# Kernel optimization log

Measured on AMD Instinct MI355X. Metric: run time of the kernel, lower is better.

Reference implementation:

```python
import jax, jax.numpy as jnp
import numpy as np

N_UNITS = 100000
N_EDGES = 1600000
NODE_DIM = 64
N_REL_TYPES = 8
LEAKY_SLOPE = 0.2


def setup_inputs() -> dict:
    key = jax.random.key(0)
    k1, k2, k3, k4, k5 = jax.random.split(key, 5)
    x_unit_base = jax.random.normal(k1, (N_UNITS, NODE_DIM), dtype=jnp.float32)
    hat_t = jax.random.normal(k2, (N_UNITS,), dtype=jnp.float32)
    a_r_params = jax.random.normal(k3, (N_REL_TYPES, 2 * NODE_DIM), dtype=jnp.float32)
    rel_edge_index = jax.random.randint(k4, (2, N_EDGES), 0, N_UNITS, dtype=jnp.int64)
    rel_edge_type = jax.random.randint(k5, (N_EDGES,), 0, N_REL_TYPES, dtype=jnp.int64)
    return {
        "x_unit_base": x_unit_base,
        "hat_t": hat_t,
        "a_r_params": a_r_params,
        "rel_edge_index": rel_edge_index,
        "rel_edge_type": rel_edge_type,
    }


def reference(x_unit_base, hat_t, a_r_params, rel_edge_index, rel_edge_type):
    n_units = x_unit_base.shape[0]
    src = rel_edge_index[0]  # [E]
    dst = rel_edge_index[1]  # [E]

    # Per-edge attention params, split into source/dest halves to avoid
    # materializing the [E, 2d] concat explicitly as a separate buffer.
    a_r = a_r_params[rel_edge_type]          # [E, 2d]
    d = x_unit_base.shape[1]
    a_u, a_v = a_r[:, :d], a_r[:, d:]
    # e = sum(a_r * cat(x_u, x_v)) = <a_u, x_u> + <a_v, x_v>
    e = jnp.sum(a_u * x_unit_base[src], axis=-1) + jnp.sum(a_v * x_unit_base[dst], axis=-1)
    e = jax.nn.leaky_relu(e, negative_slope=LEAKY_SLOPE)  # [E]

    # scatter_softmax over edges grouped by src
    seg_max = jax.ops.segment_max(e, src, num_segments=n_units)  # [N]
    ex = jnp.exp(e - seg_max[src])
    denom = jax.ops.segment_sum(ex, src, num_segments=n_units)   # [N]
    alpha = ex / denom[src]                                       # [E]

    # weighted scatter-sum of imputed treatments
    weighted_t = alpha * hat_t[dst]
    g_u = jax.ops.segment_sum(weighted_t, src, num_segments=n_units)  # [N]
    return g_u[:, None]
```

## Files before the change

### kernel.cpp

```cpp
#include <hip/hip_runtime.h>

#define LEAKY_SLOPE 0.2f
#define SHIFT 20.0f
#define CHUNK 2048
#define LG_CHUNK 11
#define NCH_MAX 64
#define EPB 4096
#define CAP_MIN 34816


__device__ __forceinline__ float lrelu_exp(float a, float b) {
    float e = a + b;
    e = (e > 0.f) ? e : LEAKY_SLOPE * e;
    return __expf(e - SHIFT);
}

template <int NC, bool FUSED>
__global__ __launch_bounds__(256) void node_table_kernel(const float* __restrict__ x,
                                                         const float* __restrict__ a,
                                                         const float* __restrict__ hat_t,
                                                         float* __restrict__ su,
                                                         float* __restrict__ svx,
                                                         float2* __restrict__ nd,
                                                         unsigned* __restrict__ gcur,
                                                         int n_units) {
    int u = blockIdx.x * blockDim.x + threadIdx.x;
    if (blockIdx.x == 0 && threadIdx.x < NCH_MAX && gcur) gcur[threadIdx.x] = 0u;
    if (u >= n_units) return;
#pragma unroll
    for (int k = 0; k < NC; ++k) nd[(size_t)k * n_units + u] = make_float2(0.f, 0.f);

    float4 xr[16];
    const float4* xp = reinterpret_cast<const float4*>(x + (size_t)u * 64);
#pragma unroll
    for (int k = 0; k < 16; ++k) xr[k] = xp[k];

    float out_u[8], out_v[8];
#pragma unroll
    for (int r = 0; r < 8; ++r) {
        const float* ar = a + r * 128;
        float au = 0.f, av = 0.f;
#pragma unroll
        for (int k = 0; k < 16; ++k) {
            float4 xk = xr[k];
            au = fmaf(ar[4 * k + 0], xk.x, au);
            au = fmaf(ar[4 * k + 1], xk.y, au);
            au = fmaf(ar[4 * k + 2], xk.z, au);
            au = fmaf(ar[4 * k + 3], xk.w, au);
            av = fmaf(ar[64 + 4 * k + 0], xk.x, av);
            av = fmaf(ar[64 + 4 * k + 1], xk.y, av);
            av = fmaf(ar[64 + 4 * k + 2], xk.z, av);
            av = fmaf(ar[64 + 4 * k + 3], xk.w, av);
        }
        out_u[r] = au;
        out_v[r] = av;
    }
    float4* sup = reinterpret_cast<float4*>(su + (size_t)u * 8);
    sup[0] = make_float4(out_u[0], out_u[1], out_u[2], out_u[3]);
    sup[1] = make_float4(out_u[4], out_u[5], out_u[6], out_u[7]);
    if (FUSED) {
        float ht = hat_t[u];
        float4* svp = reinterpret_cast<float4*>(svx + (size_t)u * 16);
        svp[0] = make_float4(out_v[0], ht, out_v[1], ht);
        svp[1] = make_float4(out_v[2], ht, out_v[3], ht);
        svp[2] = make_float4(out_v[4], ht, out_v[5], ht);
        svp[3] = make_float4(out_v[6], ht, out_v[7], ht);
    } else {
        float4* svp = reinterpret_cast<float4*>(svx + (size_t)u * 8);
        svp[0] = make_float4(out_v[0], out_v[1], out_v[2], out_v[3]);
        svp[1] = make_float4(out_v[4], out_v[5], out_v[6], out_v[7]);
    }
}

__global__ __launch_bounds__(256) void scatter_kernel(const int* __restrict__ src,
                                                      const int* __restrict__ dst,
                                                      const int* __restrict__ typ,
                                                      unsigned* __restrict__ gcur,
                                                      uint2* __restrict__ buckets,
                                                      int cap, int nch, int n_edges) {
    __shared__ unsigned lcnt[NCH_MAX];
    __shared__ unsigned lbase[NCH_MAX];
    const int tid = threadIdx.x;
    if (tid < NCH_MAX) lcnt[tid] = 0u;
    __syncthreads();

    const int base = blockIdx.x * EPB;
    unsigned pk[16], qk[16], rk[16];
#pragma unroll
    for (int r = 0; r < 4; ++r) {
        int e = base + tid * 4 + r * 1024;
        if (e + 4 <= n_edges) {
            int4 s4 = *reinterpret_cast<const int4*>(src + e);
            int4 d4 = *reinterpret_cast<const int4*>(dst + e);
            int4 t4 = *reinterpret_cast<const int4*>(typ + e);
            int ss[4] = {s4.x, s4.y, s4.z, s4.w};
            int dd[4] = {d4.x, d4.y, d4.z, d4.w};
            int tt[4] = {t4.x, t4.y, t4.z, t4.w};
#pragma unroll
            for (int i = 0; i < 4; ++i) {
                unsigned p = ((unsigned)ss[i] << 3) | (unsigned)tt[i];
                unsigned q = ((unsigned)dd[i] << 3) | (unsigned)tt[i];
                pk[r * 4 + i] = p;
                qk[r * 4 + i] = q;
                rk[r * 4 + i] = atomicAdd(&lcnt[p >> (3 + LG_CHUNK)], 1u);
            }
        }
    }
    __syncthreads();
    if (tid < nch) lbase[tid] = atomicAdd(&gcur[tid], lcnt[tid]);
    __syncthreads();
#pragma unroll
    for (int r = 0; r < 4; ++r) {
        int e = base + tid * 4 + r * 1024;
        if (e + 4 <= n_edges) {
#pragma unroll
            for (int i = 0; i < 4; ++i) {
                unsigned p = pk[r * 4 + i];
                unsigned b = p >> (3 + LG_CHUNK);
                unsigned pos = lbase[b] + rk[r * 4 + i];
                if (pos < (unsigned)cap)
                    buckets[(size_t)b * cap + pos] = make_uint2(p, qk[r * 4 + i]);
            }
        }
    }
}

__device__ __forceinline__ void accum_edge(uint2 e, const float* __restrict__ su,
                                           const float2* __restrict__ svh,
                                           float* __restrict__ lden,
                                           float* __restrict__ lnum) {
    float suv = su[e.x];
    float2 pv = svh[e.y];
    float ex = lrelu_exp(suv, pv.x);
    unsigned sl = (e.x >> 3) & (CHUNK - 1);
    atomicAdd(&lden[sl], ex);
    atomicAdd(&lnum[sl], ex * pv.y);
}

__global__ __launch_bounds__(256) void accum_kernel(const uint2* __restrict__ buckets,
                                                    const unsigned* __restrict__ gcur,
                                                    const float* __restrict__ su,
                                                    const float2* __restrict__ svh,
                                                    float2* __restrict__ partial,
                                                    int cap, int b_c) {
    __shared__ float lden[CHUNK];
    __shared__ float lnum[CHUNK];
    const int bid = blockIdx.x;
    const int c = bid / b_c;
    const int j = bid - c * b_c;
    for (int i = threadIdx.x; i < CHUNK; i += 256) { lden[i] = 0.f; lnum[i] = 0.f; }
    __syncthreads();

    int cnt = (int)gcur[c];
    if (cnt > cap) cnt = cap;
    const uint2* ep = buckets + (size_t)c * cap;
    int lo = (int)(((long)j * cnt / b_c) & ~1L);
    int hi = (j == b_c - 1) ? cnt : (int)(((long)(j + 1) * cnt / b_c) & ~1L);

    int i = lo + threadIdx.x * 2;
    for (; i + 512 + 1 < hi; i += 1024) {
        uint4 a = *reinterpret_cast<const uint4*>(ep + i);
        uint4 b = *reinterpret_cast<const uint4*>(ep + i + 512);
        accum_edge(make_uint2(a.x, a.y), su, svh, lden, lnum);
        accum_edge(make_uint2(a.z, a.w), su, svh, lden, lnum);
        accum_edge(make_uint2(b.x, b.y), su, svh, lden, lnum);
        accum_edge(make_uint2(b.z, b.w), su, svh, lden, lnum);
    }
    for (; i + 1 < hi; i += 512) {
        uint4 a = *reinterpret_cast<const uint4*>(ep + i);
        accum_edge(make_uint2(a.x, a.y), su, svh, lden, lnum);
        accum_edge(make_uint2(a.z, a.w), su, svh, lden, lnum);
    }
    if ((hi - lo) & 1) {
        if (threadIdx.x == 0) accum_edge(ep[hi - 1], su, svh, lden, lnum);
    }
    __syncthreads();
    float2* op = partial + (size_t)bid * CHUNK;
    for (int k = threadIdx.x; k < CHUNK; k += 256)
        op[k] = make_float2(lden[k], lnum[k]);
}

__global__ __launch_bounds__(256) void reduce_kernel(const float2* __restrict__ partial,
                                                     float* __restrict__ out,
                                                     int n_units, int b_c) {
    int u = blockIdx.x * blockDim.x + threadIdx.x;
    if (u >= n_units) return;
    int c = u >> LG_CHUNK;
    int idx = u & (CHUNK - 1);
    const float2* p = partial + ((size_t)c * b_c) * CHUNK + idx;
    float den = 0.f, num = 0.f;
    for (int j = 0; j < b_c; ++j) {
        float2 v = p[(size_t)j * CHUNK];
        den += v.x;
        num += v.y;
    }
    out[u] = (den > 0.f) ? num / den : 0.f;
}

__device__ __forceinline__ void pair_add_dev(float* f, float a, float b) {
    atomicAdd(f, a);
    atomicAdd(f + 1, b);
}

template <bool FUSED>
__global__ __launch_bounds__(256) void edge_sum_kernel(const int* __restrict__ src,
                                                       const int* __restrict__ dst,
                                                       const int* __restrict__ typ,
                                                       const float* __restrict__ su,
                                                       const float* __restrict__ svx,
                                                       const float* __restrict__ hat_t,
                                                       float2* __restrict__ nd,
                                                       int n_edges) {
    int e0 = (blockIdx.x * blockDim.x + threadIdx.x) * 2;
    float* ndf = (float*)nd;
    if (e0 + 1 < n_edges) {
        int2 s2 = *reinterpret_cast<const int2*>(src + e0);
        int2 d2 = *reinterpret_cast<const int2*>(dst + e0);
        int2 t2 = *reinterpret_cast<const int2*>(typ + e0);
        float su0 = su[(size_t)s2.x * 8 + t2.x];
        float su1 = su[(size_t)s2.y * 8 + t2.y];
        float sv0, sv1, ht0, ht1;
        if (FUSED) {
            const float2* svh = reinterpret_cast<const float2*>(svx);
            float2 p0 = svh[(size_t)d2.x * 8 + t2.x];
            float2 p1 = svh[(size_t)d2.y * 8 + t2.y];
            sv0 = p0.x; ht0 = p0.y;
            sv1 = p1.x; ht1 = p1.y;
        } else {
            sv0 = svx[(size_t)d2.x * 8 + t2.x];
            sv1 = svx[(size_t)d2.y * 8 + t2.y];
            ht0 = hat_t[d2.x];
            ht1 = hat_t[d2.y];
        }
        float ex0 = lrelu_exp(su0, sv0);
        float ex1 = lrelu_exp(su1, sv1);
        pair_add_dev(ndf + 2 * (size_t)s2.x, ex0, ex0 * ht0);
        pair_add_dev(ndf + 2 * (size_t)s2.y, ex1, ex1 * ht1);
    } else if (e0 < n_edges) {
        int s = src[e0], d = dst[e0], t = typ[e0];
        float sv_v, ht;
        if (FUSED) {
            float2 p = reinterpret_cast<const float2*>(svx)[(size_t)d * 8 + t];
            sv_v = p.x; ht = p.y;
        } else {
            sv_v = svx[(size_t)d * 8 + t];
            ht = hat_t[d];
        }
        float ex = lrelu_exp(su[(size_t)s * 8 + t], sv_v);
        pair_add_dev(ndf + 2 * (size_t)s, ex, ex * ht);
    }
}

__global__ __launch_bounds__(256) void finalize_kernel(const float2* __restrict__ nd,
                                                       float* __restrict__ out, int n) {
    int i = blockIdx.x * blockDim.x + threadIdx.x;
    if (i < n) {
        float2 v = nd[i];
        out[i] = (v.x > 0.f) ? v.y / v.x : 0.f;
    }
}

extern "C" void kernel_launch(void* const* d_in, const int* in_sizes, int n_in,
                              void* d_out, int out_size, void* d_ws, size_t ws_size,
                              hipStream_t stream) {
    const float* x     = (const float*)d_in[0];
    const float* hat_t = (const float*)d_in[1];
    const float* a     = (const float*)d_in[2];
    const int*   ei    = (const int*)d_in[3];
    const int*   et    = (const int*)d_in[4];

    const int n_units = in_sizes[1];
    const int n_edges = in_sizes[4];
    const int* src = ei;
    const int* dst = ei + n_edges;

    const size_t n = (size_t)n_units;
    const int B = 256;
    const int gu = (n_units + B - 1) / B;
    char* ws = (char*)d_ws;

    const int nch = (n_units + CHUNK - 1) >> LG_CHUNK;
    const size_t tab = n * 96;
    const size_t curb = 256;

    int b_c = 11;
    int cap = 0;
    for (; b_c >= 4; b_c -= 7) {
        size_t part = (size_t)nch * b_c * CHUNK * 8;
        size_t head = tab + curb + part;
        if (ws_size <= head) continue;
        cap = (int)((ws_size - head) / ((size_t)nch * 8)) & ~1;
        if (cap > 49152) cap = 49152;
        if (cap >= CAP_MIN) break;
        cap = 0;
    }

    if (cap >= CAP_MIN && nch <= NCH_MAX) {
        float* su       = (float*)ws;
        float* svx      = su + n * 8;
        unsigned* gcur  = (unsigned*)(ws + tab);
        uint2* buckets  = (uint2*)(ws + tab + curb);
        float2* partial = (float2*)(ws + tab + curb + (size_t)nch * cap * 8);
        const int gs = (n_edges + EPB - 1) / EPB;
        node_table_kernel<0, true><<<gu, B, 0, stream>>>(x, a, hat_t, su, svx, nullptr, gcur, n_units);
        scatter_kernel<<<gs, B, 0, stream>>>(src, dst, et, gcur, buckets, cap, nch, n_edges);
        accum_kernel<<<nch * b_c, B, 0, stream>>>(buckets, gcur, su, (const float2*)svx,
                                                  partial, cap, b_c);
        reduce_kernel<<<gu, B, 0, stream>>>(partial, (float*)d_out, n_units, b_c);
    } else if (ws_size >= n * 104) {
        float2* nd = (float2*)ws;
        float* su  = (float*)(ws + n * 8);
        float* svx = su + n * 8;
        const int ge = ((n_edges + 1) / 2 + B - 1) / B;
        node_table_kernel<1, true><<<gu, B, 0, stream>>>(x, a, hat_t, su, svx, nd, nullptr, n_units);
        edge_sum_kernel<true><<<ge, B, 0, stream>>>(src, dst, et, su, svx, hat_t, nd, n_edges);
        finalize_kernel<<<gu, B, 0, stream>>>(nd, (float*)d_out, n_units);
    } else {
        float2* nd = (float2*)ws;
        float* su  = (float*)(ws + n * 8);
        float* svx = su + n * 8;
        const int ge = ((n_edges + 1) / 2 + B - 1) / B;
        node_table_kernel<1, false><<<gu, B, 0, stream>>>(x, a, hat_t, su, svx, nd, nullptr, n_units);
        edge_sum_kernel<false><<<ge, B, 0, stream>>>(src, dst, et, su, svx, hat_t, nd, n_edges);
        finalize_kernel<<<gu, B, 0, stream>>>(nd, (float*)d_out, n_units);
    }
}
```

Before: 160.6 us.

## Bucket edges by source chunk and destination group with packed 32-bit entries

Edges are now bucketed by source chunk and also by a group of destination chunks, so each accumulation block gathers from a narrower range of the destination table and gets better cache locality. Each edge is packed into one 32-bit word (local source, type, destination) instead of a uint2, halving bucket traffic. The node table computation and the edge scatter are fused into one launch with disjoint block ranges, and the counter reset moves to a memset. The packing limits node count to below 2^18, and the smaller bucket capacity risks dropping edges if any bucket overflows.

New measurement: 138.3 us. -13.9%, faster.

```diff
diff --git a/kernel.cpp b/kernel.cpp
--- a/kernel.cpp
+++ b/kernel.cpp
@@ -4,9 +4,11 @@
 #define SHIFT 20.0f
 #define CHUNK 2048
 #define LG_CHUNK 11
-#define NCH_MAX 64
+#define NG 8
+#define NSL 2
+#define NB_MAX 512
 #define EPB 4096
-#define CAP_MIN 34816
+#define CAP_MIN 4608
 
 
 __device__ __forceinline__ float lrelu_exp(float a, float b) {
@@ -15,26 +17,199 @@
     return __expf(e - SHIFT);
 }
 
-template <int NC, bool FUSED>
-__global__ __launch_bounds__(256) void node_table_kernel(const float* __restrict__ x,
-                                                         const float* __restrict__ a,
-                                                         const float* __restrict__ hat_t,
-                                                         float* __restrict__ su,
-                                                         float* __restrict__ svx,
-                                                         float2* __restrict__ nd,
-                                                         unsigned* __restrict__ gcur,
-                                                         int n_units) {
+__global__ __launch_bounds__(256) void table_scatter_kernel(
+        const float* __restrict__ x, const float* __restrict__ a,
+        const float* __restrict__ hat_t,
+        const int* __restrict__ src, const int* __restrict__ dst,
+        const int* __restrict__ typ,
+        float* __restrict__ su, float* __restrict__ svx,
+        unsigned* __restrict__ gcur, unsigned* __restrict__ buckets,
+        int cap, int nch, int n_units, int n_edges, int gs) {
+    __shared__ unsigned lcnt[NB_MAX];
+    __shared__ unsigned lbase[NB_MAX];
+    const int tid = threadIdx.x;
+
+    if ((int)blockIdx.x < gs) {
+        const int nb = nch * NG;
+        for (int i = tid; i < nb; i += 256) lcnt[i] = 0u;
+        __syncthreads();
+
+        const int base = blockIdx.x * EPB;
+        unsigned ent[16], rnk[16], bkt[16];
+#pragma unroll
+        for (int r = 0; r < 4; ++r) {
+            int e = base + tid * 4 + r * 1024;
+            if (e + 4 <= n_edges) {
+                int4 s4 = *reinterpret_cast<const int4*>(src + e);
+                int4 d4 = *reinterpret_cast<const int4*>(dst + e);
+                int4 t4 = *reinterpret_cast<const int4*>(typ + e);
+                int ss[4] = {s4.x, s4.y, s4.z, s4.w};
+                int dd[4] = {d4.x, d4.y, d4.z, d4.w};
+                int tt[4] = {t4.x, t4.y, t4.z, t4.w};
+#pragma unroll
+                for (int i = 0; i < 4; ++i) {
+                    unsigned s = (unsigned)ss[i], d = (unsigned)dd[i], t = (unsigned)tt[i];
+                    unsigned b = (s >> LG_CHUNK) * NG + ((d >> LG_CHUNK) & (NG - 1));
+                    ent[r * 4 + i] = ((s & (CHUNK - 1)) << 21) | (t << 18) | d;
+                    bkt[r * 4 + i] = b;
+                    rnk[r * 4 + i] = atomicAdd(&lcnt[b], 1u);
+                }
+            } else {
+#pragma unroll
+                for (int i = 0; i < 4; ++i) {
+                    int ee = e + i;
+                    if (ee < n_edges) {
+                        unsigned s = (unsigned)src[ee], d = (unsigned)dst[ee], t = (unsigned)typ[ee];
+                        unsigned b = (s >> LG_CHUNK) * NG + ((d >> LG_CHUNK) & (NG - 1));
+                        ent[r * 4 + i] = ((s & (CHUNK - 1)) << 21) | (t << 18) | d;
+                        bkt[r * 4 + i] = b;
+                        rnk[r * 4 + i] = atomicAdd(&lcnt[b], 1u);
+                    } else {
+                        bkt[r * 4 + i] = 0xFFFFFFFFu;
+                    }
+                }
+            }
+        }
+        __syncthreads();
+        for (int i = tid; i < nb; i += 256)
+            lbase[i] = lcnt[i] ? atomicAdd(&gcur[i], lcnt[i]) : 0u;
+        __syncthreads();
+#pragma unroll
+        for (int k = 0; k < 16; ++k) {
+            unsigned b = bkt[k];
+            if (b != 0xFFFFFFFFu) {
+                unsigned pos = lbase[b] + rnk[k];
+                if (pos < (unsigned)cap)
+                    buckets[(size_t)b * cap + pos] = ent[k];
+            }
+        }
+    } else {
+        int u = ((int)blockIdx.x - gs) * 256 + tid;
+        if (u >= n_units) return;
+        float4 xr[16];
+        const float4* xp = reinterpret_cast<const float4*>(x + (size_t)u * 64);
+#pragma unroll
+        for (int k = 0; k < 16; ++k) xr[k] = xp[k];
+
+        float out_u[8], out_v[8];
+#pragma unroll
+        for (int r = 0; r < 8; ++r) {
+            const float* ar = a + r * 128;
+            float au = 0.f, av = 0.f;
+#pragma unroll
+            for (int k = 0; k < 16; ++k) {
+                float4 xk = xr[k];
+                au = fmaf(ar[4 * k + 0], xk.x, au);
+                au = fmaf(ar[4 * k + 1], xk.y, au);
+                au = fmaf(ar[4 * k + 2], xk.z, au);
+                au = fmaf(ar[4 * k + 3], xk.w, au);
+                av = fmaf(ar[64 + 4 * k + 0], xk.x, av);
+                av = fmaf(ar[64 + 4 * k + 1], xk.y, av);
+                av = fmaf(ar[64 + 4 * k + 2], xk.z, av);
+                av = fmaf(ar[64 + 4 * k + 3], xk.w, av);
+            }
+            out_u[r] = au;
+            out_v[r] = av;
+        }
+        float4* sup = reinterpret_cast<float4*>(su + (size_t)u * 8);
+        sup[0] = make_float4(out_u[0], out_u[1], out_u[2], out_u[3]);
+        sup[1] = make_float4(out_u[4], out_u[5], out_u[6], out_u[7]);
+        float ht = hat_t[u];
+        float4* svp = reinterpret_cast<float4*>(svx + (size_t)u * 16);
+        svp[0] = make_float4(out_v[0], ht, out_v[1], ht);
+        svp[1] = make_float4(out_v[2], ht, out_v[3], ht);
+        svp[2] = make_float4(out_v[4], ht, out_v[5], ht);
+        svp[3] = make_float4(out_v[6], ht, out_v[7], ht);
+    }
+}
+
+__device__ __forceinline__ void accum_edge(unsigned e, const float* __restrict__ suc,
+                                           const float2* __restrict__ svh,
+                                           float* __restrict__ lden,
+                                           float* __restrict__ lnum) {
+    unsigned s_l = e >> 21;
+    unsigned t = (e >> 18) & 7u;
+    unsigned d = e & 0x3FFFFu;
+    float suv = suc[(s_l << 3) | t];
+    float2 pv = svh[((size_t)d << 3) | t];
+    float ex = lrelu_exp(suv, pv.x);
+    atomicAdd(&lden[s_l], ex);
+    atomicAdd(&lnum[s_l], ex * pv.y);
+}
+
+__global__ __launch_bounds__(256) void accum_kernel(const unsigned* __restrict__ buckets,
+                                                    const unsigned* __restrict__ gcur,
+                                                    const float* __restrict__ su,
+                                                    const float2* __restrict__ svh,
+                                                    float2* __restrict__ partial,
+                                                    int cap) {
+    __shared__ float lden[CHUNK];
+    __shared__ float lnum[CHUNK];
+    const int bid = blockIdx.x;
+    const int g = bid & (NG - 1);
+    const int rest = bid >> 3;
+    const int sl = rest & (NSL - 1);
+    const int c = rest >> 1;
+    for (int i = threadIdx.x; i < CHUNK; i += 256) { lden[i] = 0.f; lnum[i] = 0.f; }
+    __syncthreads();
+
+    const int b = c * NG + g;
+    int cnt = (int)gcur[b];
+    if (cnt > cap) cnt = cap;
+    const unsigned* ep = buckets + (size_t)b * cap;
+    int lo = (sl * cnt / NSL) & ~3;
+    int hi = (sl == NSL - 1) ? cnt : (((sl + 1) * cnt / NSL) & ~3);
+    const float* suc = su + (((size_t)c << LG_CHUNK) << 3);
+
+    for (int i = lo + threadIdx.x * 4; i + 4 <= hi; i += 1024) {
+        uint4 q = *reinterpret_cast<const uint4*>(ep + i);
+        accum_edge(q.x, suc, svh, lden, lnum);
+        accum_edge(q.y, suc, svh, lden, lnum);
+        accum_edge(q.z, suc, svh, lden, lnum);
+        accum_edge(q.w, suc, svh, lden, lnum);
+    }
+    int rem = (hi - lo) & 3;
+    if ((int)threadIdx.x < rem) accum_edge(ep[hi - rem + threadIdx.x], suc, svh, lden, lnum);
+
+    __syncthreads();
+    float2* op = partial + (size_t)bid * CHUNK;
+    for (int k = threadIdx.x; k < CHUNK; k += 256)
+        op[k] = make_float2(lden[k], lnum[k]);
+}
+
+__global__ __launch_bounds__(256) void reduce_kernel(const float2* __restrict__ partial,
+                                                     float* __restrict__ out,
+                                                     int n_units) {
     int u = blockIdx.x * blockDim.x + threadIdx.x;
-    if (blockIdx.x == 0 && threadIdx.x < NCH_MAX && gcur) gcur[threadIdx.x] = 0u;
     if (u >= n_units) return;
-#pragma unroll
-    for (int k = 0; k < NC; ++k) nd[(size_t)k * n_units + u] = make_float2(0.f, 0.f);
-
+    int c = u >> LG_CHUNK;
+    int i = u & (CHUNK - 1);
+    const float2* p = partial + ((size_t)c * (NSL * NG)) * CHUNK + i;
+    float den = 0.f, num = 0.f;
+#pragma unroll
+    for (int k = 0; k < NSL * NG; ++k) {
+        float2 v = p[(size_t)k * CHUNK];
+        den += v.x;
+        num += v.y;
+    }
+    out[u] = (den > 0.f) ? num / den : 0.f;
+}
+
+template <bool FUSED>
+__global__ __launch_bounds__(256) void node_table_fb_kernel(const float* __restrict__ x,
+                                                            const float* __restrict__ a,
+                                                            const float* __restrict__ hat_t,
+                                                            float* __restrict__ su,
+                                                            float* __restrict__ svx,
+                                                            float2* __restrict__ nd,
+                                                            int n_units) {
+    int u = blockIdx.x * blockDim.x + threadIdx.x;
+    if (u >= n_units) return;
+    nd[u] = make_float2(0.f, 0.f);
     float4 xr[16];
     const float4* xp = reinterpret_cast<const float4*>(x + (size_t)u * 64);
 #pragma unroll
     for (int k = 0; k < 16; ++k) xr[k] = xp[k];
-
     float out_u[8], out_v[8];
 #pragma unroll
     for (int r = 0; r < 8; ++r) {
@@ -70,131 +245,6 @@
         svp[0] = make_float4(out_v[0], out_v[1], out_v[2], out_v[3]);
         svp[1] = make_float4(out_v[4], out_v[5], out_v[6], out_v[7]);
     }
-}
-
-__global__ __launch_bounds__(256) void scatter_kernel(const int* __restrict__ src,
-                                                      const int* __restrict__ dst,
-                                                      const int* __restrict__ typ,
-                                                      unsigned* __restrict__ gcur,
-                                                      uint2* __restrict__ buckets,
-                                                      int cap, int nch, int n_edges) {
-    __shared__ unsigned lcnt[NCH_MAX];
-    __shared__ unsigned lbase[NCH_MAX];
-    const int tid = threadIdx.x;
-    if (tid < NCH_MAX) lcnt[tid] = 0u;
-    __syncthreads();
-
-    const int base = blockIdx.x * EPB;
-    unsigned pk[16], qk[16], rk[16];
-#pragma unroll
-    for (int r = 0; r < 4; ++r) {
-        int e = base + tid * 4 + r * 1024;
-        if (e + 4 <= n_edges) {
-            int4 s4 = *reinterpret_cast<const int4*>(src + e);
-            int4 d4 = *reinterpret_cast<const int4*>(dst + e);
-            int4 t4 = *reinterpret_cast<const int4*>(typ + e);
-            int ss[4] = {s4.x, s4.y, s4.z, s4.w};
-            int dd[4] = {d4.x, d4.y, d4.z, d4.w};
-            int tt[4] = {t4.x, t4.y, t4.z, t4.w};
-#pragma unroll
-            for (int i = 0; i < 4; ++i) {
-                unsigned p = ((unsigned)ss[i] << 3) | (unsigned)tt[i];
-                unsigned q = ((unsigned)dd[i] << 3) | (unsigned)tt[i];
-                pk[r * 4 + i] = p;
-                qk[r * 4 + i] = q;
-                rk[r * 4 + i] = atomicAdd(&lcnt[p >> (3 + LG_CHUNK)], 1u);
-            }
-        }
-    }
-    __syncthreads();
-    if (tid < nch) lbase[tid] = atomicAdd(&gcur[tid], lcnt[tid]);
-    __syncthreads();
-#pragma unroll
-    for (int r = 0; r < 4; ++r) {
-        int e = base + tid * 4 + r * 1024;
-        if (e + 4 <= n_edges) {
-#pragma unroll
-            for (int i = 0; i < 4; ++i) {
-                unsigned p = pk[r * 4 + i];
-                unsigned b = p >> (3 + LG_CHUNK);
-                unsigned pos = lbase[b] + rk[r * 4 + i];
-                if (pos < (unsigned)cap)
-                    buckets[(size_t)b * cap + pos] = make_uint2(p, qk[r * 4 + i]);
-            }
-        }
-    }
-}
-
-__device__ __forceinline__ void accum_edge(uint2 e, const float* __restrict__ su,
-                                           const float2* __restrict__ svh,
-                                           float* __restrict__ lden,
-                                           float* __restrict__ lnum) {
-    float suv = su[e.x];
-    float2 pv = svh[e.y];
-    float ex = lrelu_exp(suv, pv.x);
-    unsigned sl = (e.x >> 3) & (CHUNK - 1);
-    atomicAdd(&lden[sl], ex);
-    atomicAdd(&lnum[sl], ex * pv.y);
-}
-
-__global__ __launch_bounds__(256) void accum_kernel(const uint2* __restrict__ buckets,
-                                                    const unsigned* __restrict__ gcur,
-                                                    const float* __restrict__ su,
-                                                    const float2* __restrict__ svh,
-                                                    float2* __restrict__ partial,
-                                                    int cap, int b_c) {
-    __shared__ float lden[CHUNK];
-    __shared__ float lnum[CHUNK];
-    const int bid = blockIdx.x;
-    const int c = bid / b_c;
-    const int j = bid - c * b_c;
-    for (int i = threadIdx.x; i < CHUNK; i += 256) { lden[i] = 0.f; lnum[i] = 0.f; }
-    __syncthreads();
-
-    int cnt = (int)gcur[c];
-    if (cnt > cap) cnt = cap;
-    const uint2* ep = buckets + (size_t)c * cap;
-    int lo = (int)(((long)j * cnt / b_c) & ~1L);
-    int hi = (j == b_c - 1) ? cnt : (int)(((long)(j + 1) * cnt / b_c) & ~1L);
-
-    int i = lo + threadIdx.x * 2;
-    for (; i + 512 + 1 < hi; i += 1024) {
-        uint4 a = *reinterpret_cast<const uint4*>(ep + i);
-        uint4 b = *reinterpret_cast<const uint4*>(ep + i + 512);
-        accum_edge(make_uint2(a.x, a.y), su, svh, lden, lnum);
-        accum_edge(make_uint2(a.z, a.w), su, svh, lden, lnum);
-        accum_edge(make_uint2(b.x, b.y), su, svh, lden, lnum);
-        accum_edge(make_uint2(b.z, b.w), su, svh, lden, lnum);
-    }
-    for (; i + 1 < hi; i += 512) {
-        uint4 a = *reinterpret_cast<const uint4*>(ep + i);
-        accum_edge(make_uint2(a.x, a.y), su, svh, lden, lnum);
-        accum_edge(make_uint2(a.z, a.w), su, svh, lden, lnum);
-    }
-    if ((hi - lo) & 1) {
-        if (threadIdx.x == 0) accum_edge(ep[hi - 1], su, svh, lden, lnum);
-    }
-    __syncthreads();
-    float2* op = partial + (size_t)bid * CHUNK;
-    for (int k = threadIdx.x; k < CHUNK; k += 256)
-        op[k] = make_float2(lden[k], lnum[k]);
-}
-
-__global__ __launch_bounds__(256) void reduce_kernel(const float2* __restrict__ partial,
-                                                     float* __restrict__ out,
-                                                     int n_units, int b_c) {
-    int u = blockIdx.x * blockDim.x + threadIdx.x;
-    if (u >= n_units) return;
-    int c = u >> LG_CHUNK;
-    int idx = u & (CHUNK - 1);
-    const float2* p = partial + ((size_t)c * b_c) * CHUNK + idx;
-    float den = 0.f, num = 0.f;
-    for (int j = 0; j < b_c; ++j) {
-        float2 v = p[(size_t)j * CHUNK];
-        den += v.x;
-        num += v.y;
-    }
-    out[u] = (den > 0.f) ? num / den : 0.f;
 }
 
 __device__ __forceinline__ void pair_add_dev(float* f, float a, float b) {
@@ -280,39 +330,42 @@
     char* ws = (char*)d_ws;
 
     const int nch = (n_units + CHUNK - 1) >> LG_CHUNK;
+    const int nb = nch * NG;
     const size_t tab = n * 96;
-    const size_t curb = 256;
-
-    int b_c = 11;
+    const size_t curb = 4096;
+    const size_t partb = (size_t)nch * NSL * NG * CHUNK * 8;
+
     int cap = 0;
-    for (; b_c >= 4; b_c -= 7) {
-        size_t part = (size_t)nch * b_c * CHUNK * 8;
-        size_t head = tab + curb + part;
-        if (ws_size <= head) continue;
-        cap = (int)((ws_size - head) / ((size_t)nch * 8)) & ~1;
-        if (cap > 49152) cap = 49152;
-        if (cap >= CAP_MIN) break;
-        cap = 0;
-    }
-
-    if (cap >= CAP_MIN && nch <= NCH_MAX) {
+    if (nb <= NB_MAX && n_units < (1 << 18)) {
+        size_t head = tab + curb + partb;
+        if (ws_size > head) {
+            cap = (int)((ws_size - head) / ((size_t)nb * 4)) & ~3;
+            if (cap > 8192) cap = 8192;
+            if (cap < CAP_MIN) cap = 0;
+        }
+    }
+
+    if (cap > 0) {
         float* su       = (float*)ws;
         float* svx      = su + n * 8;
         unsigned* gcur  = (unsigned*)(ws + tab);
-        uint2* buckets  = (uint2*)(ws + tab + curb);
-        float2* partial = (float2*)(ws + tab + curb + (size_t)nch * cap * 8);
+        unsigned* buckets = (unsigned*)(ws + tab + curb);
+        float2* partial = (float2*)(ws + tab + curb + (size_t)nb * cap * 4);
         const int gs = (n_edges + EPB - 1) / EPB;
-        node_table_kernel<0, true><<<gu, B, 0, stream>>>(x, a, hat_t, su, svx, nullptr, gcur, n_units);
-        scatter_kernel<<<gs, B, 0, stream>>>(src, dst, et, gcur, buckets, cap, nch, n_edges);
-        accum_kernel<<<nch * b_c, B, 0, stream>>>(buckets, gcur, su, (const float2*)svx,
-                                                  partial, cap, b_c);
-        reduce_kernel<<<gu, B, 0, stream>>>(partial, (float*)d_out, n_units, b_c);
+
+        hipMemsetAsync(gcur, 0, (size_t)nb * 4, stream);
+        table_scatter_kernel<<<gs + gu, B, 0, stream>>>(x, a, hat_t, src, dst, et,
+                                                        su, svx, gcur, buckets,
+                                                        cap, nch, n_units, n_edges, gs);
+        accum_kernel<<<nch * NSL * NG, B, 0, stream>>>(buckets, gcur, su,
+                                                       (const float2*)svx, partial, cap);
+        reduce_kernel<<<gu, B, 0, stream>>>(partial, (float*)d_out, n_units);
     } else if (ws_size >= n * 104) {
         float2* nd = (float2*)ws;
         float* su  = (float*)(ws + n * 8);
         float* svx = su + n * 8;
         const int ge = ((n_edges + 1) / 2 + B - 1) / B;
-        node_table_kernel<1, true><<<gu, B, 0, stream>>>(x, a, hat_t, su, svx, nd, nullptr, n_units);
+        node_table_fb_kernel<true><<<gu, B, 0, stream>>>(x, a, hat_t, su, svx, nd, n_units);
         edge_sum_kernel<true><<<ge, B, 0, stream>>>(src, dst, et, su, svx, hat_t, nd, n_edges);
         finalize_kernel<<<gu, B, 0, stream>>>(nd, (float*)d_out, n_units);
     } else {
@@ -320,7 +373,7 @@
         float* su  = (float*)(ws + n * 8);
         float* svx = su + n * 8;
         const int ge = ((n_edges + 1) / 2 + B - 1) / B;
-        node_table_kernel<1, false><<<gu, B, 0, stream>>>(x, a, hat_t, su, svx, nd, nullptr, n_units);
+        node_table_fb_kernel<false><<<gu, B, 0, stream>>>(x, a, hat_t, su, svx, nd, n_units);
         edge_sum_kernel<false><<<ge, B, 0, stream>>>(src, dst, et, su, svx, hat_t, nd, n_edges);
         finalize_kernel<<<gu, B, 0, stream>>>(nd, (float*)d_out, n_units);
     }
```
